# Kernel tuning notes

Measured on AMD Instinct MI355X. Metric: run time of the kernel, lower is better.

Reference implementation:

```python
import jax, jax.numpy as jnp
import numpy as np

B, L, E, H, D = 32, 512, 256, 8, 64
SCALE = int(D ** 0.5)  # matches TF: int(hidden_dim ** 0.5) == 8


def setup_inputs() -> dict:
    key = jax.random.key(0)
    ks = jax.random.split(key, 6)
    return {
        "x": jax.random.normal(ks[0], (B, L, E), dtype=jnp.float32),
        "positional": jax.random.normal(ks[1], (L, E), dtype=jnp.float32) * 0.02,
        "Wq": jax.random.normal(ks[2], (H, E, D), dtype=jnp.float32) * 0.05,
        "Wk": jax.random.normal(ks[3], (H, E, D), dtype=jnp.float32) * 0.05,
        "Wv": jax.random.normal(ks[4], (H, E, D), dtype=jnp.float32) * 0.05,
        "Wo": jax.random.normal(ks[5], (H * D, E), dtype=jnp.float32) * 0.05,
    }


def reference(x, positional, Wq, Wk, Wv, Wo):
    act = jnp.tanh  # activation='tanh'
    xp = x + positional                                   # [B,L,E]
    # Batched per-head projections with activation applied post-matmul
    q = act(jnp.einsum('ble,hed->bhld', xp, Wq))          # [B,H,L,D]
    k = act(jnp.einsum('ble,hed->bhld', xp, Wk))
    v = act(jnp.einsum('ble,hed->bhld', xp, Wv))
    score = jnp.einsum('bhqd,bhkd->bhqk', q, k) / SCALE   # [B,H,L,L]
    attn = jax.nn.softmax(score, axis=-1)
    out = jnp.einsum('bhqk,bhkd->bhqd', attn, v)          # [B,H,L,D]
    # concat heads along last axis (head-major) -> [B,L,H*D]
    out = jnp.transpose(out, (0, 2, 1, 3)).reshape(B, L, H * D)
    return jnp.einsum('blf,fe->ble', out, Wo) + act(xp)   # [B,L,E]
```

## Files before the change

### kernel.cpp

```cpp
#include <hip/hip_runtime.h>
#include <cstdint>

#define NB 32
#define NL 512
#define NE 256
#define NH 8
#define ND 64
#define NM 16384
#define NHD 512

using half8  = __attribute__((ext_vector_type(8))) _Float16;
using half4  = __attribute__((ext_vector_type(4))) _Float16;
using f32x4  = __attribute__((ext_vector_type(4))) float;
using f32x16 = __attribute__((ext_vector_type(16))) float;

__device__ __forceinline__ f32x4 mfma16(half8 a, half8 b, f32x4 c) {
    return __builtin_amdgcn_mfma_f32_16x16x32_f16(a, b, c, 0, 0, 0);
}
__device__ __forceinline__ f32x16 mfma32(half8 a, half8 b, f32x16 c) {
    return __builtin_amdgcn_mfma_f32_32x32x16_f16(a, b, c, 0, 0, 0);
}
__device__ __forceinline__ void cp16_g2l(const void* g, void* l) {
    __builtin_amdgcn_global_load_lds(
        (const __attribute__((address_space(1))) void*)g,
        (__attribute__((address_space(3))) void*)l, 16, 0, 0);
}
__device__ __forceinline__ float fast_tanh(float x) {
    float xc = fminf(fmaxf(x, -9.f), 9.f);
    float t = __expf(2.f * xc);
    return (t - 1.f) * __builtin_amdgcn_rcpf(t + 1.f);
}

__global__ __launch_bounds__(256) void prep(
        const float* __restrict__ x, const float* __restrict__ pos,
        const float* __restrict__ Wq, const float* __restrict__ Wk,
        const float* __restrict__ Wv, const float* __restrict__ Wo,
        _Float16* __restrict__ wqkv, _Float16* __restrict__ woh,
        _Float16* __restrict__ xph) {
    int bid = blockIdx.x;
    if (bid < 2048) {
        int idx = bid * 256 + threadIdx.x;
        if (idx < 1536 * 256) {
            int n = idx >> 8, e = idx & 255;
            int s = n >> 9, h = (n >> 6) & 7, d = n & 63;
            const float* W = (s == 0) ? Wq : (s == 1) ? Wk : Wv;
            wqkv[idx] = (_Float16)W[(h * NE + e) * ND + d];
        } else {
            int j = idx - 1536 * 256;
            int e = j >> 9, f = j & 511;
            woh[j] = (_Float16)Wo[f * NE + e];
        }
    } else {
        int i = ((bid - 2048) * 256 + threadIdx.x) * 4;
        float4 xv = *(const float4*)(x + i);
        float4 pv = *(const float4*)(pos + (i & (NL * NE - 1)));
        half4 o;
        o[0] = (_Float16)(xv.x + pv.x);
        o[1] = (_Float16)(xv.y + pv.y);
        o[2] = (_Float16)(xv.z + pv.z);
        o[3] = (_Float16)(xv.w + pv.w);
        *(half4*)(xph + i) = o;
    }
}

__global__ __launch_bounds__(256) void proj_gemm(
        const _Float16* __restrict__ wqkv, const _Float16* __restrict__ xph,
        _Float16* __restrict__ q_all, _Float16* __restrict__ k_all,
        _Float16* __restrict__ vT) {
    __shared__ _Float16 Alds[2][128 * 64];
    __shared__ _Float16 Blds[2][128 * 64];
    int tid = threadIdx.x;
    int w = tid >> 6, l = tid & 63;
    int bid = blockIdx.x;
    int xcd = bid & 7, local = bid >> 3;
    int tn = local % 12;
    int tm = xcd * 16 + local / 12;
    int wn = w >> 1, wm = w & 1;
    int m16 = l & 15, g = l >> 4;
    bool isv = (tn >= 8);
    int lrow8 = l >> 3;
    int kc16 = (l & 7) ^ lrow8;
    f32x4 acc[4][4] = {};

    const _Float16* Ag = wqkv + (size_t)tn * 128 * 256;
    const _Float16* Bg = xph + (size_t)tm * 128 * 256;

#define PROJ_STAGE(kt, buf)                                                   \
    _Pragma("unroll") for (int i = 0; i < 4; ++i) {                           \
        int cA = w * 4 + i;                                                   \
        int row = cA * 8 + lrow8;                                             \
        cp16_g2l(Ag + (size_t)row * 256 + (kt) * 64 + kc16 * 8,               \
                 &Alds[buf][cA * 512]);                                       \
        cp16_g2l(Bg + (size_t)row * 256 + (kt) * 64 + kc16 * 8,               \
                 &Blds[buf][cA * 512]);                                       \
    }

    PROJ_STAGE(0, 0);
    __syncthreads();
    int cur = 0;
    for (int kt = 0; kt < 4; ++kt) {
        if (kt < 3) { PROJ_STAGE(kt + 1, cur ^ 1); }
#pragma unroll
        for (int ks = 0; ks < 2; ++ks) {
            half8 af[4], bf[4];
#pragma unroll
            for (int f = 0; f < 4; ++f) {
                int ra = wn * 64 + f * 16 + m16;
                int rb = wm * 64 + f * 16 + m16;
                af[f] = *(const half8*)(&Alds[cur][ra * 64 + (((ks * 4 + g) ^ (ra & 7)) << 3)]);
                bf[f] = *(const half8*)(&Blds[cur][rb * 64 + (((ks * 4 + g) ^ (rb & 7)) << 3)]);
            }
            if (!isv) {
#pragma unroll
                for (int nf = 0; nf < 4; ++nf)
#pragma unroll
                    for (int mf = 0; mf < 4; ++mf)
                        acc[nf][mf] = mfma16(af[nf], bf[mf], acc[nf][mf]);
            } else {
#pragma unroll
                for (int nf = 0; nf < 4; ++nf)
#pragma unroll
                    for (int mf = 0; mf < 4; ++mf)
                        acc[nf][mf] = mfma16(bf[mf], af[nf], acc[nf][mf]);
            }
        }
        __syncthreads();
        cur ^= 1;
    }
#undef PROJ_STAGE
    if (!isv) {
        _Float16* dst = (tn < 4) ? q_all : k_all;
#pragma unroll
        for (int nf = 0; nf < 4; ++nf) {
            int c = (tn & 3) * 128 + wn * 64 + nf * 16 + g * 4;
#pragma unroll
            for (int mf = 0; mf < 4; ++mf) {
                int m = tm * 128 + wm * 64 + mf * 16 + m16;
                f32x4 v = acc[nf][mf];
                half4 hv;
#pragma unroll
                for (int r = 0; r < 4; ++r) hv[r] = (_Float16)fast_tanh(v[r]);
                *(half4*)(dst + (size_t)m * NHD + c) = hv;
            }
        }
    } else {
#pragma unroll
        for (int nf = 0; nf < 4; ++nf) {
            int c = (tn - 8) * 128 + wn * 64 + nf * 16 + m16;
#pragma unroll
            for (int mf = 0; mf < 4; ++mf) {
                int t0 = tm * 128 + wm * 64 + mf * 16 + g * 4;
                f32x4 v = acc[nf][mf];
                half4 hv;
#pragma unroll
                for (int r = 0; r < 4; ++r) hv[r] = (_Float16)fast_tanh(v[r]);
                *(half4*)(vT + (size_t)c * NM + t0) = hv;
            }
        }
    }
}

__global__ __launch_bounds__(256, 3) void attn_kernel(
        const _Float16* __restrict__ q_all, const _Float16* __restrict__ k_all,
        const _Float16* __restrict__ vT, _Float16* __restrict__ attn_out) {
    __shared__ _Float16 Klds[2][64 * 64];
    __shared__ _Float16 Vtlds[2][64 * 64];
    __shared__ _Float16 Plds[4][32 * 64];
    int tid = threadIdx.x;
    int w = tid >> 6, l = tid & 63;
    int l31 = l & 31, hi = l >> 5;
    int bid = blockIdx.x;
    int qt = bid & 3, h = (bid >> 2) & 7, b = bid >> 5;

    int qbase = qt * 128 + w * 32;
    half8 qf[4];
    {
        const _Float16* qp = q_all + (size_t)(b * NL + qbase + l31) * NHD + h * ND + hi * 8;
#pragma unroll
        for (int ks = 0; ks < 4; ++ks) qf[ks] = *(const half8*)(qp + ks * 16);
    }

    f32x16 acc_o[2] = {};
    float mrow = -1e30f, lrow = 0.f;

    int st_row = tid >> 2;
    int st_u0 = (tid & 3) * 2;
    const _Float16* kg = k_all + (size_t)(b * NL + st_row) * NHD + h * ND + st_u0 * 8;
    const _Float16* vg = vT + (size_t)(h * ND + st_row) * NM + b * NL + st_u0 * 8;
    int so0 = st_row * 64 + ((st_u0 ^ (st_row & 7)) << 3);
    int so1 = st_row * 64 + (((st_u0 + 1) ^ (st_row & 7)) << 3);

    uint4 kv0 = *(const uint4*)(kg);
    uint4 kv1 = *(const uint4*)(kg + 8);
    uint4 vv0 = *(const uint4*)(vg);
    uint4 vv1 = *(const uint4*)(vg + 8);
    *(uint4*)&Klds[0][so0] = kv0;   *(uint4*)&Klds[0][so1] = kv1;
    *(uint4*)&Vtlds[0][so0] = vv0;  *(uint4*)&Vtlds[0][so1] = vv1;
    __syncthreads();

    for (int kt = 0; kt < 8; ++kt) {
        int cur = kt & 1;
        if (kt < 7) {
            const _Float16* kp = kg + (size_t)(kt + 1) * 64 * NHD;
            const _Float16* vp = vg + (kt + 1) * 64;
            kv0 = *(const uint4*)(kp);      kv1 = *(const uint4*)(kp + 8);
            vv0 = *(const uint4*)(vp);      vv1 = *(const uint4*)(vp + 8);
        }
        f32x16 acc_s[2] = {};
        __builtin_amdgcn_s_setprio(1);
#pragma unroll
        for (int ks = 0; ks < 4; ++ks)
#pragma unroll
            for (int kb2 = 0; kb2 < 2; ++kb2) {
                int key = kb2 * 32 + l31;
                half8 kb = *(const half8*)(&Klds[cur][key * 64 + (((ks * 2 + hi) ^ (key & 7)) << 3)]);
                acc_s[kb2] = mfma32(kb, qf[ks], acc_s[kb2]);
            }
        __builtin_amdgcn_s_setprio(0);
        float mx = -1e30f;
#pragma unroll
        for (int kb2 = 0; kb2 < 2; ++kb2)
#pragma unroll
            for (int j = 0; j < 16; ++j) mx = fmaxf(mx, acc_s[kb2][j]);
        mx = fmaxf(mx, __shfl_xor(mx, 32));
        mx *= 0.125f;
        if (!__all(mx <= mrow + 8.f)) {
            float mn = fmaxf(mrow, mx);
            float alpha = __expf(mrow - mn);
            mrow = mn;
            lrow *= alpha;
            float aq[16];
#pragma unroll
            for (int c = 0; c < 4; ++c)
#pragma unroll
                for (int r = 0; r < 4; ++r)
                    aq[c * 4 + r] = __shfl(alpha, c * 8 + hi * 4 + r);
#pragma unroll
            for (int d2 = 0; d2 < 2; ++d2)
#pragma unroll
                for (int j = 0; j < 16; ++j) acc_o[d2][j] *= aq[j];
        }
        float rs = 0.f;
#pragma unroll
        for (int kb2 = 0; kb2 < 2; ++kb2)
#pragma unroll
            for (int c = 0; c < 4; ++c) {
                half4 hv;
#pragma unroll
                for (int r = 0; r < 4; ++r) {
                    float p = __expf(acc_s[kb2][c * 4 + r] * 0.125f - mrow);
                    rs += p;
                    hv[r] = (_Float16)p;
                }
                int u = kb2 * 4 + c;
                *(half4*)(&Plds[w][l31 * 64 + ((u ^ (l31 & 7)) << 3) + hi * 4]) = hv;
            }
        rs += __shfl_xor(rs, 32);
        lrow += rs;
        __builtin_amdgcn_s_setprio(1);
#pragma unroll
        for (int ks = 0; ks < 4; ++ks) {
            half8 pa = *(const half8*)(&Plds[w][l31 * 64 + (((ks * 2 + hi) ^ (l31 & 7)) << 3)]);
#pragma unroll
            for (int d2 = 0; d2 < 2; ++d2) {
                int d = d2 * 32 + l31;
                half8 vb = *(const half8*)(&Vtlds[cur][d * 64 + (((ks * 2 + hi) ^ (d & 7)) << 3)]);
                acc_o[d2] = mfma32(pa, vb, acc_o[d2]);
            }
        }
        __builtin_amdgcn_s_setprio(0);
        if (kt < 7) {
            int nxt = cur ^ 1;
            *(uint4*)&Klds[nxt][so0] = kv0;   *(uint4*)&Klds[nxt][so1] = kv1;
            *(uint4*)&Vtlds[nxt][so0] = vv0;  *(uint4*)&Vtlds[nxt][so1] = vv1;
            __syncthreads();
        }
    }
    size_t orow0 = (size_t)(b * NL + qbase);
#pragma unroll
    for (int c = 0; c < 4; ++c)
#pragma unroll
        for (int r = 0; r < 4; ++r) {
            int qrow = c * 8 + hi * 4 + r;
            float inv = 1.f / __shfl(lrow, qrow);
#pragma unroll
            for (int d2 = 0; d2 < 2; ++d2)
                attn_out[(orow0 + qrow) * NHD + h * ND + d2 * 32 + l31] =
                    (_Float16)(acc_o[d2][c * 4 + r] * inv);
        }
}

__global__ __launch_bounds__(256) void final_gemm(
        const _Float16* __restrict__ woh, const _Float16* __restrict__ attn,
        const _Float16* __restrict__ xph, float* __restrict__ out) {
    __shared__ _Float16 Alds[2][128 * 64];
    __shared__ _Float16 Blds[2][64 * 64];
    int tid = threadIdx.x;
    int w = tid >> 6, l = tid & 63;
    int tn = blockIdx.x & 1, tm = blockIdx.x >> 1;
    int wn = w >> 1, wm = w & 1;
    int m16 = l & 15, g = l >> 4;
    int lrow8 = l >> 3;
    int kc16 = (l & 7) ^ lrow8;
    f32x4 acc[4][2] = {};

    const _Float16* Ag = woh + (size_t)tn * 128 * 512;
    const _Float16* Bg = attn + (size_t)tm * 64 * 512;

#define FIN_STAGE(kt, buf)                                                    \
    _Pragma("unroll") for (int i = 0; i < 4; ++i) {                           \
        int cA = w * 4 + i;                                                   \
        int row = cA * 8 + lrow8;                                             \
        cp16_g2l(Ag + (size_t)row * 512 + (kt) * 64 + kc16 * 8,               \
                 &Alds[buf][cA * 512]);                                       \
    }                                                                         \
    _Pragma("unroll") for (int i = 0; i < 2; ++i) {                           \
        int cB = w * 2 + i;                                                   \
        int row = cB * 8 + lrow8;                                             \
        cp16_g2l(Bg + (size_t)row * 512 + (kt) * 64 + kc16 * 8,               \
                 &Blds[buf][cB * 512]);                                       \
    }

    FIN_STAGE(0, 0);
    __syncthreads();
    int cur = 0;
    for (int kt = 0; kt < 8; ++kt) {
        if (kt < 7) { FIN_STAGE(kt + 1, cur ^ 1); }
#pragma unroll
        for (int ks = 0; ks < 2; ++ks) {
            half8 af[4], bf[2];
#pragma unroll
            for (int f = 0; f < 4; ++f) {
                int ra = wn * 64 + f * 16 + m16;
                af[f] = *(const half8*)(&Alds[cur][ra * 64 + (((ks * 4 + g) ^ (ra & 7)) << 3)]);
            }
#pragma unroll
            for (int f = 0; f < 2; ++f) {
                int rb = wm * 32 + f * 16 + m16;
                bf[f] = *(const half8*)(&Blds[cur][rb * 64 + (((ks * 4 + g) ^ (rb & 7)) << 3)]);
            }
#pragma unroll
            for (int nf = 0; nf < 4; ++nf)
#pragma unroll
                for (int mf = 0; mf < 2; ++mf)
                    acc[nf][mf] = mfma16(af[nf], bf[mf], acc[nf][mf]);
        }
        __syncthreads();
        cur ^= 1;
    }
#undef FIN_STAGE
#pragma unroll
    for (int nf = 0; nf < 4; ++nf) {
        int e = tn * 128 + wn * 64 + nf * 16 + g * 4;
#pragma unroll
        for (int mf = 0; mf < 2; ++mf) {
            int m = tm * 64 + wm * 32 + mf * 16 + m16;
            half4 hx = *(const half4*)(xph + (size_t)m * NE + e);
            f32x4 v = acc[nf][mf];
            float4 o;
            o.x = v[0] + fast_tanh((float)hx[0]);
            o.y = v[1] + fast_tanh((float)hx[1]);
            o.z = v[2] + fast_tanh((float)hx[2]);
            o.w = v[3] + fast_tanh((float)hx[3]);
            *(float4*)(out + (size_t)m * NE + e) = o;
        }
    }
}

extern "C" void kernel_launch(void* const* d_in, const int* in_sizes, int n_in,
                              void* d_out, int out_size, void* d_ws, size_t ws_size,
                              hipStream_t stream) {
    const float* x   = (const float*)d_in[0];
    const float* pos = (const float*)d_in[1];
    const float* Wq  = (const float*)d_in[2];
    const float* Wk  = (const float*)d_in[3];
    const float* Wv  = (const float*)d_in[4];
    const float* Wo  = (const float*)d_in[5];
    float* out = (float*)d_out;

    char* ws = (char*)d_ws;
    _Float16* xph   = (_Float16*)(ws);
    _Float16* wqkv  = (_Float16*)(ws + 8388608);
    _Float16* woh   = (_Float16*)(ws + 9175040);
    _Float16* q_all = (_Float16*)(ws + 9437184);
    _Float16* k_all = (_Float16*)(ws + 26214400);
    _Float16* vT    = (_Float16*)(ws + 42991616);
    _Float16* attn  = (_Float16*)(ws + 59768832);

    prep<<<dim3(6144), dim3(256), 0, stream>>>(x, pos, Wq, Wk, Wv, Wo, wqkv, woh, xph);
    proj_gemm<<<dim3(12 * 128), dim3(256), 0, stream>>>(wqkv, xph, q_all, k_all, vT);
    attn_kernel<<<dim3(1024), dim3(256), 0, stream>>>(q_all, k_all, vT, attn);
    final_gemm<<<dim3(512), dim3(256), 0, stream>>>(woh, attn, xph, out);
}
```

Measured before the change: 86.85 us.

## Keep softmax probabilities in registers via permlane32 swap instead of LDS round-trip

Removes the per-wave P shared-memory buffer. The S accumulator layout is converted into the MFMA A-operand layout in registers using packed fp16 conversion and permlane32_swap. This avoids the LDS writes and reads and the LDS footprint of Plds, which may also help occupancy. Exponentials are also moved to base-2 exp2 with the scale folded into an FMA, and the tanh activation uses exp2 as well. The risk is that the register permutation mapping is subtle, and round-toward-zero fp16 conversion slightly changes numerics.

```diff
diff --git a/kernel.cpp b/kernel.cpp
--- a/kernel.cpp
+++ b/kernel.cpp
@@ -13,6 +13,7 @@
 using half4  = __attribute__((ext_vector_type(4))) _Float16;
 using f32x4  = __attribute__((ext_vector_type(4))) float;
 using f32x16 = __attribute__((ext_vector_type(16))) float;
+using u32x2  = __attribute__((ext_vector_type(2))) unsigned int;
 
 __device__ __forceinline__ f32x4 mfma16(half8 a, half8 b, f32x4 c) {
     return __builtin_amdgcn_mfma_f32_16x16x32_f16(a, b, c, 0, 0, 0);
@@ -25,10 +26,17 @@
         (const __attribute__((address_space(1))) void*)g,
         (__attribute__((address_space(3))) void*)l, 16, 0, 0);
 }
+__device__ __forceinline__ float exp2fast(float x) {
+    return __builtin_amdgcn_exp2f(x);
+}
 __device__ __forceinline__ float fast_tanh(float x) {
     float xc = fminf(fmaxf(x, -9.f), 9.f);
-    float t = __expf(2.f * xc);
+    float t = exp2fast(xc * 2.88539008178f);
     return (t - 1.f) * __builtin_amdgcn_rcpf(t + 1.f);
+}
+__device__ __forceinline__ uint32_t pk16(float a, float b) {
+    auto h2 = __builtin_amdgcn_cvt_pkrtz(a, b);
+    return __builtin_bit_cast(uint32_t, h2);
 }
 
 __global__ __launch_bounds__(256) void prep(
@@ -165,12 +173,12 @@
         const _Float16* __restrict__ vT, _Float16* __restrict__ attn_out) {
     __shared__ _Float16 Klds[2][64 * 64];
     __shared__ _Float16 Vtlds[2][64 * 64];
-    __shared__ _Float16 Plds[4][32 * 64];
     int tid = threadIdx.x;
     int w = tid >> 6, l = tid & 63;
     int l31 = l & 31, hi = l >> 5;
     int bid = blockIdx.x;
     int qt = bid & 3, h = (bid >> 2) & 7, b = bid >> 5;
+    const float C1 = 0.125f * 1.44269504089f;
 
     int qbase = qt * 128 + w * 32;
     half8 qf[4];
@@ -226,7 +234,7 @@
         mx *= 0.125f;
         if (!__all(mx <= mrow + 8.f)) {
             float mn = fmaxf(mrow, mx);
-            float alpha = __expf(mrow - mn);
+            float alpha = exp2fast((mrow - mn) * 1.44269504089f);
             mrow = mn;
             lrow *= alpha;
             float aq[16];
@@ -240,32 +248,38 @@
 #pragma unroll
                 for (int j = 0; j < 16; ++j) acc_o[d2][j] *= aq[j];
         }
+        float ml = mrow * 1.44269504089f;
         float rs = 0.f;
+        uint32_t cw[2][4][2];
 #pragma unroll
         for (int kb2 = 0; kb2 < 2; ++kb2)
 #pragma unroll
-            for (int c = 0; c < 4; ++c) {
-                half4 hv;
-#pragma unroll
-                for (int r = 0; r < 4; ++r) {
-                    float p = __expf(acc_s[kb2][c * 4 + r] * 0.125f - mrow);
-                    rs += p;
-                    hv[r] = (_Float16)p;
+            for (int a = 0; a < 4; ++a)
+#pragma unroll
+                for (int p = 0; p < 2; ++p) {
+                    float p0 = exp2fast(fmaf(acc_s[kb2][4 * a + 2 * p],     C1, -ml));
+                    float p1 = exp2fast(fmaf(acc_s[kb2][4 * a + 2 * p + 1], C1, -ml));
+                    rs += p0 + p1;
+                    cw[kb2][a][p] = pk16(p0, p1);
                 }
-                int u = kb2 * 4 + c;
-                *(half4*)(&Plds[w][l31 * 64 + ((u ^ (l31 & 7)) << 3) + hi * 4]) = hv;
-            }
         rs += __shfl_xor(rs, 32);
         lrow += rs;
         __builtin_amdgcn_s_setprio(1);
 #pragma unroll
         for (int ks = 0; ks < 4; ++ks) {
-            half8 pa = *(const half8*)(&Plds[w][l31 * 64 + (((ks * 2 + hi) ^ (l31 & 7)) << 3)]);
+            int kb2 = ks >> 1, s = ks & 1;
+            u32x2 r0 = __builtin_amdgcn_permlane32_swap(
+                cw[kb2][2 * s][0], cw[kb2][2 * s + 1][0], false, false);
+            u32x2 r1 = __builtin_amdgcn_permlane32_swap(
+                cw[kb2][2 * s][1], cw[kb2][2 * s + 1][1], false, false);
+            union { uint32_t u[4]; half8 h; } pu;
+            pu.u[0] = r0[0];  pu.u[1] = r1[0];
+            pu.u[2] = r0[1];  pu.u[3] = r1[1];
 #pragma unroll
             for (int d2 = 0; d2 < 2; ++d2) {
                 int d = d2 * 32 + l31;
                 half8 vb = *(const half8*)(&Vtlds[cur][d * 64 + (((ks * 2 + hi) ^ (d & 7)) << 3)]);
-                acc_o[d2] = mfma32(pa, vb, acc_o[d2]);
+                acc_o[d2] = mfma32(pu.h, vb, acc_o[d2]);
             }
         }
         __builtin_amdgcn_s_setprio(0);
```

Measured after the change: 85.36 us. No clear change (-1.7%).
